# Kernel optimization log

Hardware: AMD Instinct MI355X
Metric: run time of the kernel (lower is better)

The kernel has to match this reference:

```python
import jax, jax.numpy as jnp
import numpy as np

RATIOS = [0.9, 0.7, 0.5, 0.3]
EPS = 1e-5


def _layernorm(x, g, b):
    m = jnp.mean(x, axis=-1, keepdims=True)
    v = jnp.mean(jnp.square(x - m), axis=-1, keepdims=True)
    return (x - m) * jax.lax.rsqrt(v + EPS) * g + b


def _stage(x, g, b, W, bias):
    return _layernorm(x, g, b) @ W + bias


def _prune(x, W1, b1, W2, b2, ratio):
    B, N, C = x.shape
    stats = jnp.mean(x, axis=1)                       # (B, C)
    scores = jax.nn.relu(stats @ W1 + b1) @ W2 + b2    # (B, C)
    k = max(1, int(C * ratio))
    _, idx = jax.lax.top_k(jax.lax.stop_gradient(scores), k)  # (B, k)
    hard = jnp.zeros((B, C), scores.dtype).at[jnp.arange(B)[:, None], idx].set(1.0)
    soft = jax.nn.sigmoid(scores)
    # straight-through: forward value == hard, gradient flows through soft
    mask = hard + soft - jax.lax.stop_gradient(soft)
    return x * mask[:, None, :]


def setup_inputs() -> dict:
    key = jax.random.key(0)
    dims = [(96, 96), (96, 192), (192, 384), (384, 768)]
    inp = {}
    ks = jax.random.split(key, 64)
    ki = iter(ks)
    inp["x"] = jax.random.normal(next(ki), (32, 3136, 96), dtype=jnp.float32)
    for i, (din, dout) in enumerate(dims, 1):
        inp[f"s{i}_g"] = jnp.ones((din,), jnp.float32)
        inp[f"s{i}_b"] = jnp.zeros((din,), jnp.float32)
        inp[f"s{i}_W"] = jax.random.normal(next(ki), (din, dout), jnp.float32) * 0.02
        inp[f"s{i}_bias"] = jnp.zeros((dout,), jnp.float32)
        d = dout
        inp[f"p{i}_W1"] = jax.random.normal(next(ki), (d, d // 4), jnp.float32) * 0.02
        inp[f"p{i}_b1"] = jnp.zeros((d // 4,), jnp.float32)
        inp[f"p{i}_W2"] = jax.random.normal(next(ki), (d // 4, d), jnp.float32) * 0.02
        inp[f"p{i}_b2"] = jnp.zeros((d,), jnp.float32)
    inp["H"] = 56
    inp["W"] = 56
    return inp


def reference(x,
              s1_g, s1_b, s1_W, s1_bias, p1_W1, p1_b1, p1_W2, p1_b2,
              s2_g, s2_b, s2_W, s2_bias, p2_W1, p2_b1, p2_W2, p2_b2,
              s3_g, s3_b, s3_W, s3_bias, p3_W1, p3_b1, p3_W2, p3_b2,
              s4_g, s4_b, s4_W, s4_bias, p4_W1, p4_b1, p4_W2, p4_b2,
              H, W):
    x = _stage(x, s1_g, s1_b, s1_W, s1_bias)
    x = _prune(x, p1_W1, p1_b1, p1_W2, p1_b2, RATIOS[0])
    x = _stage(x, s2_g, s2_b, s2_W, s2_bias)
    x = _prune(x, p2_W1, p2_b1, p2_W2, p2_b2, RATIOS[1])
    x = _stage(x, s3_g, s3_b, s3_W, s3_bias)
    x = _prune(x, p3_W1, p3_b1, p3_W2, p3_b2, RATIOS[2])
    x = _stage(x, s4_g, s4_b, s4_W, s4_bias)
    x = _prune(x, p4_W1, p4_b1, p4_W2, p4_b2, RATIOS[3])
    return x
```

## Files before the change

### kernel.cpp

```cpp
#include <hip/hip_runtime.h>
#include <hip/hip_bf16.h>
#include <stdint.h>

#define NTOK 3136
#define MTOT 100352
#define RPW  14
#define WPB  224

typedef __attribute__((ext_vector_type(8))) short bf16x8;
typedef __attribute__((ext_vector_type(4))) float f32x4;
typedef __attribute__((ext_vector_type(2))) float f32x2;

static __device__ __forceinline__ ushort f2bf(float x) {
  union { float f; uint32_t u; } c; c.f = x;
  uint32_t r = (c.u + 0x7FFFu + ((c.u >> 16) & 1u)) >> 16;
  return (ushort)r;
}
static __device__ __forceinline__ float bf2f(ushort h) {
  union { uint32_t u; float f; } c; c.u = ((uint32_t)h) << 16;
  return c.f;
}

template<int DIN, bool WLO>
__global__ __launch_bounds__(256)
void ln_colsum_k(const float* __restrict__ in, const float* __restrict__ gma,
                 const float* __restrict__ bta, ushort* __restrict__ oh,
                 ushort* __restrict__ ol, float* __restrict__ part)
{
  constexpr int P2 = DIN / 2;
  constexpr int T2 = (P2 + 63) / 64;
  const int wid  = (blockIdx.x * 256 + threadIdx.x) >> 6;
  const int lane = threadIdx.x & 63;
  const int b = wid / WPB;
  const int w = wid - b * WPB;

  f32x2 gv[T2], bv[T2], acc[T2];
#pragma unroll
  for (int t = 0; t < T2; ++t) {
    int c2 = lane + 64 * t;
    if (c2 < P2) {
      gv[t] = *(const f32x2*)(gma + 2 * c2);
      bv[t] = *(const f32x2*)(bta + 2 * c2);
    } else { gv[t] = {0.f, 0.f}; bv[t] = {0.f, 0.f}; }
    acc[t] = {0.f, 0.f};
  }

  const size_t rbase = ((size_t)b * NTOK + (size_t)w * RPW) * DIN;
  const float* ip = in + rbase;
  ushort* oph = oh + rbase;
  ushort* opl = ol + rbase;

  for (int j = 0; j < RPW; ++j) {
    f32x2 v[T2];
    float s = 0.f, sq = 0.f;
#pragma unroll
    for (int t = 0; t < T2; ++t) {
      int c2 = lane + 64 * t;
      f32x2 xv = {0.f, 0.f};
      if (c2 < P2) xv = *(const f32x2*)(ip + (size_t)j * DIN + 2 * c2);
      v[t] = xv;
      s  += xv[0] + xv[1];
      sq += xv[0] * xv[0] + xv[1] * xv[1];
    }
#pragma unroll
    for (int off = 1; off < 64; off <<= 1) {
      s  += __shfl_xor(s, off);
      sq += __shfl_xor(sq, off);
    }
    float m   = s / (float)DIN;
    float var = sq / (float)DIN - m * m;
    float r   = 1.f / sqrtf(var + 1e-5f);
#pragma unroll
    for (int t = 0; t < T2; ++t) {
      int c2 = lane + 64 * t;
      if (c2 < P2) {
        float xn0 = (v[t][0] - m) * r * gv[t][0] + bv[t][0];
        float xn1 = (v[t][1] - m) * r * gv[t][1] + bv[t][1];
        ushort h0 = f2bf(xn0), h1 = f2bf(xn1);
        ((uint32_t*)(oph + (size_t)j * DIN))[c2] =
            (uint32_t)h0 | ((uint32_t)h1 << 16);
        if (WLO) {
          ushort l0 = f2bf(xn0 - bf2f(h0)), l1 = f2bf(xn1 - bf2f(h1));
          ((uint32_t*)(opl + (size_t)j * DIN))[c2] =
              (uint32_t)l0 | ((uint32_t)l1 << 16);
        }
        acc[t][0] += xn0;
        acc[t][1] += xn1;
      }
    }
  }
#pragma unroll
  for (int t = 0; t < T2; ++t) {
    int c2 = lane + 64 * t;
    if (c2 < P2) {
      int c = 2 * c2;
      part[((size_t)b * DIN + c) * WPB + w]     = acc[t][0];
      part[((size_t)b * DIN + c + 1) * WPB + w] = acc[t][1];
    }
  }
}

template<int DIN, int DOUT, int SLOTS, bool CMP>
__global__ __launch_bounds__(1024)
void scores_k(const float* __restrict__ part,
              const float* __restrict__ Wt, const float* __restrict__ bias,
              const float* __restrict__ W1, const float* __restrict__ b1,
              const float* __restrict__ W2, const float* __restrict__ b2,
              float* __restrict__ mask, int k,
              const ushort* __restrict__ wsrc, ushort* __restrict__ wc,
              int* __restrict__ list_g, float* __restrict__ biasc)
{
  constexpr int DH  = DOUT / 4;
  constexpr int DH4 = DH / 4;
  constexpr int NSLC = (1024 / DH4 < 64) ? 1024 / DH4 : 64;
  constexpr int RPSC = (DOUT + NSLC - 1) / NSLC;
  constexpr int C4  = DOUT / 4;
  constexpr int NSLD = (1024 / C4 < 64) ? 1024 / C4 : 64;
  constexpr int RPSD = (DH + NSLD - 1) / NSLD;

  __shared__ float xm[DIN];
  __shared__ float st[DOUT];
  __shared__ float h[DH];
  __shared__ float sc[DOUT];
  __shared__ float red[4096];
  __shared__ int lsh[256];

  const int b = blockIdx.x, tid = threadIdx.x;

  if constexpr (SLOTS == 25) {
    if (tid < DIN) {
      const float* p = part + ((size_t)b * DIN + tid) * 25;
      float s = 0.f;
#pragma unroll
      for (int i = 0; i < 25; ++i) s += p[i];
      xm[tid] = s * (1.f / (float)NTOK);
    }
  } else {
    const int cg = tid >> 2, wq = tid & 3;
    if (cg < DIN) {
      const float* p = part + ((size_t)b * DIN + cg) * WPB + wq * 56;
      f32x4 a = {0.f, 0.f, 0.f, 0.f};
#pragma unroll
      for (int u = 0; u < 14; ++u) {
        f32x4 t0 = *(const f32x4*)(p + u * 4);
        a[0] += t0[0]; a[1] += t0[1]; a[2] += t0[2]; a[3] += t0[3];
      }
      red[wq * DIN + cg] = (a[0] + a[1]) + (a[2] + a[3]);
    }
    __syncthreads();
    if (tid < DIN)
      xm[tid] = ((red[0 * DIN + tid] + red[1 * DIN + tid]) +
                 (red[2 * DIN + tid] + red[3 * DIN + tid])) * (1.f / (float)NTOK);
  }
  __syncthreads();

  {
    constexpr int RPS = DIN / 4;
    const int j4 = tid % C4, sl = tid / C4;
    if (sl < 4) {
      const float* wp = Wt + (size_t)(sl * RPS) * DOUT + j4 * 4;
      f32x4 acc = {0.f, 0.f, 0.f, 0.f};
#pragma unroll
      for (int r = 0; r < RPS; ++r) {
        f32x4 wv = *(const f32x4*)(wp + (size_t)r * DOUT);
        float xv = xm[sl * RPS + r];
        acc[0] = fmaf(xv, wv[0], acc[0]);
        acc[1] = fmaf(xv, wv[1], acc[1]);
        acc[2] = fmaf(xv, wv[2], acc[2]);
        acc[3] = fmaf(xv, wv[3], acc[3]);
      }
      *(f32x4*)&red[sl * DOUT + j4 * 4] = acc;
    }
  }
  __syncthreads();
  if (tid < DOUT)
    st[tid] = ((red[0 * DOUT + tid] + red[1 * DOUT + tid]) +
               (red[2 * DOUT + tid] + red[3 * DOUT + tid])) + bias[tid];
  __syncthreads();

  {
    const int j4 = tid % DH4, sl = tid / DH4;
    if (sl < NSLC) {
      f32x4 acc = {0.f, 0.f, 0.f, 0.f};
#pragma unroll
      for (int rr = 0; rr < RPSC; ++rr) {
        int r = sl * RPSC + rr;
        if (r < DOUT) {
          f32x4 wv = *(const f32x4*)(W1 + (size_t)r * DH + j4 * 4);
          float sv = st[r];
          acc[0] = fmaf(sv, wv[0], acc[0]);
          acc[1] = fmaf(sv, wv[1], acc[1]);
          acc[2] = fmaf(sv, wv[2], acc[2]);
          acc[3] = fmaf(sv, wv[3], acc[3]);
        }
      }
      *(f32x4*)&red[(size_t)sl * DH + j4 * 4] = acc;
    }
  }
  __syncthreads();
  if (tid < DH) {
    float a = 0.f;
#pragma unroll 4
    for (int sl = 0; sl < NSLC; ++sl) a += red[(size_t)sl * DH + tid];
    h[tid] = fmaxf(b1[tid] + a, 0.f);
  }
  __syncthreads();

  {
    const int c4 = tid % C4, sl = tid / C4;
    if (sl < NSLD) {
      f32x4 acc = {0.f, 0.f, 0.f, 0.f};
#pragma unroll
      for (int rr = 0; rr < RPSD; ++rr) {
        int r = sl * RPSD + rr;
        if (r < DH) {
          f32x4 wv = *(const f32x4*)(W2 + (size_t)r * DOUT + c4 * 4);
          float hv = h[r];
          acc[0] = fmaf(hv, wv[0], acc[0]);
          acc[1] = fmaf(hv, wv[1], acc[1]);
          acc[2] = fmaf(hv, wv[2], acc[2]);
          acc[3] = fmaf(hv, wv[3], acc[3]);
        }
      }
      *(f32x4*)&red[(size_t)sl * DOUT + c4 * 4] = acc;
    }
  }
  __syncthreads();
  for (int c = tid; c < DOUT; c += 1024) {
    float a = 0.f;
#pragma unroll 4
    for (int sl = 0; sl < NSLD; ++sl) a += red[(size_t)sl * DOUT + c];
    sc[c] = b2[c] + a;
  }
  __syncthreads();

  for (int c = tid; c < DOUT; c += 1024) {
    float v = sc[c];
    int rank = 0;
#pragma unroll 8
    for (int j = 0; j < DOUT; ++j) {
      float u = sc[j];
      rank += (u > v) || (u == v && j < c);
    }
    mask[(size_t)b * DOUT + c] = (rank < k) ? 1.f : 0.f;
    if (CMP && rank < k) lsh[rank] = c;
  }
  if constexpr (CMP) {
    if (tid >= k && tid < 256) lsh[tid] = -1;
    __syncthreads();
    if (tid < 256) {
      int c = lsh[tid];
      list_g[b * 256 + tid] = c;
      biasc[b * 256 + tid] = (c >= 0) ? bias[c] : 0.f;
    }
    constexpr int U4 = 384 / 8;
    for (int idx = tid; idx < 256 * U4; idx += 1024) {
      int j = idx / U4, u = idx - j * U4;
      int src = lsh[j];
      uint4 v = make_uint4(0u, 0u, 0u, 0u);
      if (src >= 0) v = *(const uint4*)(wsrc + (size_t)src * 384 + u * 8);
      *(uint4*)(wc + (size_t)b * 98304 + (size_t)j * 384 + u * 8) = v;
    }
  }
}

__global__ __launch_bounds__(256)
void convW_all_k(const float* __restrict__ W0, const float* __restrict__ W1,
                 const float* __restrict__ W2, const float* __restrict__ W3,
                 ushort* __restrict__ hi, ushort* __restrict__ lo)
{
  const int Kd[4]   = { 96, 96, 192, 384 };
  const int Nd[4]   = { 96, 192, 384, 768 };
  const int off[5]  = { 0, 12288, 36864, 110592, 405504 };
  const float* Wp[4] = { W0, W1, W2, W3 };

  int idx = blockIdx.x * 256 + threadIdx.x;
  if (idx >= 405504) return;
  int s = (idx >= off[1]) + (idx >= off[2]) + (idx >= off[3]);
  int local = idx - off[s];
  int K = Kd[s], N = Nd[s];
  int n = local / K, kk = local - n * K;
  float v = (n < N) ? Wp[s][(size_t)kk * N + n] : 0.f;
  ushort h = f2bf(v);
  hi[idx] = h;
  lo[idx] = f2bf(v - bf2f(h));
}

#define ASYNC16(GP, LP) __builtin_amdgcn_global_load_lds( \
    (const __attribute__((address_space(1))) void*)(GP),  \
    (__attribute__((address_space(3))) void*)(LP), 16, 0, 0)

template<int K, int NSEG, int BNL, int N, int NWN, bool WLO>
__global__ __launch_bounds__(128 * NWN)
void gemm_ln_k(const ushort* __restrict__ a0, const ushort* __restrict__ a1,
               const ushort* __restrict__ a2,
               const ushort* __restrict__ b0, const ushort* __restrict__ b1,
               const ushort* __restrict__ b2,
               const float* __restrict__ bias, const float* __restrict__ msk,
               const float* __restrict__ gnext, const float* __restrict__ bnext,
               ushort* __restrict__ oh, ushort* __restrict__ ol,
               float* __restrict__ part)
{
  constexpr int T   = 128 * NWN;
  constexpr int R   = T / 4;
  constexpr int AI  = 128 / R;
  constexpr int BI  = BNL / R;
  constexpr int IS  = AI + BI;
  constexpr int WN  = N / NWN;
  constexpr int NFR = WN / 16;
  constexpr int KSTEPS = K / 32;
  constexpr int NT  = NSEG * KSTEPS;
  __shared__ __align__(16) ushort ldsA[3][128 * 32];
  __shared__ __align__(16) ushort ldsB[3][BNL * 32];

  const int tid  = threadIdx.x;
  const int lane = tid & 63;
  const int wid  = tid >> 6;
  const int wm = wid & 1, wn = wid >> 1;

  const int q8  = gridDim.x >> 3;
  const int bid = blockIdx.x;
  const int mt  = (bid & 7) * q8 + (bid >> 3);
  const size_t row0 = (size_t)mt * 128;

  const ushort* Aseg[3] = { a0, a1, a2 };
  const ushort* Bseg[3] = { b0, b1, b2 };

  f32x4 acc[4][NFR];
#pragma unroll
  for (int i = 0; i < 4; ++i)
#pragma unroll
    for (int j = 0; j < NFR; ++j) acc[i][j] = { 0.f, 0.f, 0.f, 0.f };

  const int c_row  = tid >> 2;
  const int c_phys = tid & 3;

#define STAGEF(BUF, TT)                                                        \
  {                                                                            \
    const int seg_ = (TT) / KSTEPS;                                            \
    const int k0_  = ((TT) % KSTEPS) * 32;                                     \
    const ushort* ap_ = Aseg[seg_];                                            \
    const ushort* bp_ = Bseg[seg_];                                            \
    _Pragma("unroll")                                                          \
    for (int r_ = 0; r_ < AI; ++r_) {                                          \
      int row_  = c_row + r_ * R;                                              \
      int slot_ = c_phys ^ ((row_ >> 1) & 3);                                  \
      ASYNC16(ap_ + (row0 + row_) * (size_t)K + (k0_ + slot_ * 8),             \
              &ldsA[BUF][(row_ * 4 + c_phys) * 8]);                            \
    }                                                                          \
    _Pragma("unroll")                                                          \
    for (int r_ = 0; r_ < BI; ++r_) {                                          \
      int row_  = c_row + r_ * R;                                              \
      int slot_ = c_phys ^ ((row_ >> 1) & 3);                                  \
      ASYNC16(bp_ + (size_t)row_ * K + (k0_ + slot_ * 8),                      \
              &ldsB[BUF][(row_ * 4 + c_phys) * 8]);                            \
    }                                                                          \
  }

  STAGEF(0, 0);
  STAGEF(1, 1);
#pragma unroll
  for (int t = 0; t < NT; ++t) {
    if (t == NT - 1)            { asm volatile("s_waitcnt vmcnt(0)" ::: "memory"); }
    else if constexpr (IS == 4) { asm volatile("s_waitcnt vmcnt(4)" ::: "memory"); }
    else                        { asm volatile("s_waitcnt vmcnt(5)" ::: "memory"); }
    __builtin_amdgcn_s_barrier();
    if (t + 2 < NT) STAGEF((t + 2) % 3, t + 2);
    const int buf = t % 3;
    const int slot = lane >> 4;
    const int r16  = lane & 15;
    bf16x8 af[4], bfr[NFR];
#pragma unroll
    for (int mi = 0; mi < 4; ++mi) {
      int r = wm * 64 + mi * 16 + r16;
      af[mi] = *(const bf16x8*)&ldsA[buf][(r * 4 + (slot ^ ((r >> 1) & 3))) * 8];
    }
#pragma unroll
    for (int ni = 0; ni < NFR; ++ni) {
      int r = wn * WN + ni * 16 + r16;
      bfr[ni] = *(const bf16x8*)&ldsB[buf][(r * 4 + (slot ^ ((r >> 1) & 3))) * 8];
    }
#pragma unroll
    for (int mi = 0; mi < 4; ++mi)
#pragma unroll
      for (int ni = 0; ni < NFR; ++ni)
        acc[mi][ni] = __builtin_amdgcn_mfma_f32_16x16x32_bf16(af[mi], bfr[ni],
                                                              acc[mi][ni], 0, 0, 0);
  }
#undef STAGEF

  __syncthreads();

  float* rowred = (float*)&ldsA[0][0];
  ushort* xsh = (ushort*)&ldsB[0][0];
  ushort* xsl = xsh + 32 * N;
  float* colred = (float*)(xsh + 32 * N * (WLO ? 2 : 1));

  const int l15 = lane & 15, l4 = lane >> 4;
  const int b0i = (int)(row0 / NTOK);
  const size_t rowB = (size_t)(b0i + 1) * NTOK;
  const bool strad = rowB < row0 + 128;

  float biasv[NFR], mk0a[NFR], mk1a[NFR], gvn[NFR], bvn[NFR];
#pragma unroll
  for (int ni = 0; ni < NFR; ++ni) {
    int n = wn * WN + ni * 16 + l15;
    biasv[ni] = bias[n];
    mk0a[ni] = msk[(size_t)b0i * N + n];
    mk1a[ni] = strad ? msk[(size_t)(b0i + 1) * N + n] : mk0a[ni];
    gvn[ni] = gnext[n];
    bvn[ni] = bnext[n];
  }

  float rs[16], rq[16];
#pragma unroll
  for (int i = 0; i < 16; ++i) { rs[i] = 0.f; rq[i] = 0.f; }
#pragma unroll
  for (int mi = 0; mi < 4; ++mi)
#pragma unroll
    for (int q = 0; q < 4; ++q) {
      size_t row = row0 + wm * 64 + mi * 16 + l4 * 4 + q;
      bool loB = row < rowB;
#pragma unroll
      for (int ni = 0; ni < NFR; ++ni) {
        float v = (acc[mi][ni][q] + biasv[ni]) * (loB ? mk0a[ni] : mk1a[ni]);
        acc[mi][ni][q] = v;
        rs[mi * 4 + q] += v;
        rq[mi * 4 + q] += v * v;
      }
    }
#pragma unroll
  for (int off = 1; off < 16; off <<= 1)
#pragma unroll
    for (int i = 0; i < 16; ++i) {
      rs[i] += __shfl_xor(rs[i], off);
      rq[i] += __shfl_xor(rq[i], off);
    }
  if (l15 == 0) {
#pragma unroll
    for (int mi = 0; mi < 4; ++mi)
#pragma unroll
      for (int q = 0; q < 4; ++q) {
        int r = wm * 64 + mi * 16 + l4 * 4 + q;
        rowred[(wn * 128 + r) * 2 + 0] = rs[mi * 4 + q];
        rowred[(wn * 128 + r) * 2 + 1] = rq[mi * 4 + q];
      }
  }
  __syncthreads();

  float mean[16], rstd[16];
#pragma unroll
  for (int mi = 0; mi < 4; ++mi)
#pragma unroll
    for (int q = 0; q < 4; ++q) {
      int r = wm * 64 + mi * 16 + l4 * 4 + q;
      float S = 0.f, Q = 0.f;
#pragma unroll
      for (int w = 0; w < NWN; ++w) {
        S += rowred[(w * 128 + r) * 2 + 0];
        Q += rowred[(w * 128 + r) * 2 + 1];
      }
      float mn  = S / (float)N;
      float var = Q / (float)N - mn * mn;
      mean[mi * 4 + q] = mn;
      rstd[mi * 4 + q] = 1.f / sqrtf(var + 1e-5f);
    }

  float cs0[NFR], cs1[NFR];
#pragma unroll
  for (int ni = 0; ni < NFR; ++ni) { cs0[ni] = 0.f; cs1[ni] = 0.f; }
#pragma unroll
  for (int mi = 0; mi < 4; ++mi) {
    __syncthreads();
#pragma unroll
    for (int q = 0; q < 4; ++q) {
      const int rl = l4 * 4 + q;
      const size_t row = row0 + wm * 64 + mi * 16 + rl;
      const bool loB = row < rowB;
      const float mn = mean[mi * 4 + q], rv = rstd[mi * 4 + q];
#pragma unroll
      for (int ni = 0; ni < NFR; ++ni) {
        const int n = wn * WN + ni * 16 + l15;
        float xn = (acc[mi][ni][q] - mn) * rv * gvn[ni] + bvn[ni];
        ushort hh = f2bf(xn);
        xsh[(wm * 16 + rl) * N + n] = hh;
        if constexpr (WLO) xsl[(wm * 16 + rl) * N + n] = f2bf(xn - bf2f(hh));
        if (loB) cs0[ni] += xn; else cs1[ni] += xn;
      }
    }
    __syncthreads();
    constexpr int U4R = N / 8;
    for (int idx = tid; idx < 32 * U4R; idx += T) {
      const int grp = idx / U4R, c = idx - grp * U4R;
      const size_t row = row0 + (grp >> 4) * 64 + mi * 16 + (grp & 15);
      *(uint4*)(oh + row * (size_t)N + c * 8) =
          *(const uint4*)(xsh + grp * N + c * 8);
      if constexpr (WLO)
        *(uint4*)(ol + row * (size_t)N + c * 8) =
            *(const uint4*)(xsl + grp * N + c * 8);
    }
  }

#pragma unroll
  for (int ni = 0; ni < NFR; ++ni) {
    cs0[ni] += __shfl_xor(cs0[ni], 16);
    cs0[ni] += __shfl_xor(cs0[ni], 32);
    cs1[ni] += __shfl_xor(cs1[ni], 16);
    cs1[ni] += __shfl_xor(cs1[ni], 32);
  }
  __syncthreads();
  if (l4 == 0) {
#pragma unroll
    for (int ni = 0; ni < NFR; ++ni) {
      int n = wn * WN + ni * 16 + l15;
      colred[(0 * 2 + wm) * N + n] = cs0[ni];
      colred[(1 * 2 + wm) * N + n] = cs1[ni];
    }
  }
  __syncthreads();
  if (wm == 0 && l4 == 0) {
    const int mt_lo = (b0i * NTOK) >> 7;
    const int slot0 = mt - mt_lo;
#pragma unroll
    for (int ni = 0; ni < NFR; ++ni) {
      int n = wn * WN + ni * 16 + l15;
      float t0 = colred[0 * N + n] + colred[1 * N + n];
      part[((size_t)b0i * N + n) * 25 + slot0] = t0;
      if (strad) {
        float t1 = colred[2 * N + n] + colred[3 * N + n];
        part[((size_t)(b0i + 1) * N + n) * 25 + 0] = t1;
      }
    }
  }
}

template<int K>
__global__ __launch_bounds__(512)
void gemm_c4_k(const ushort* __restrict__ A, const ushort* __restrict__ Wc,
               const int* __restrict__ list, const float* __restrict__ biasc,
               float* __restrict__ C)
{
  constexpr int NT = K / 32;
  __shared__ __align__(16) ushort ldsA[3][128 * 32];
  __shared__ __align__(16) ushort ldsB[3][256 * 32];

  const int tid  = threadIdx.x;
  const int lane = tid & 63;
  const int wid  = tid >> 6;
  const int wm = wid & 1, wn = wid >> 1;

  const int q8  = gridDim.x >> 3;
  const int bid = blockIdx.x;
  const int wg  = (bid & 7) * q8 + (bid >> 3);
  const int b   = wg / 25;
  const int mt  = wg - b * 25;
  const size_t row0 = (size_t)b * NTOK + (size_t)mt * 128;
  const int rows_valid = (mt == 24) ? 64 : 128;

  const ushort* bp = Wc + (size_t)b * 256 * K;

  const int c_row  = tid >> 2;
  const int c_phys = tid & 3;

  size_t arow = row0 + c_row;
  const size_t rowEnd = (size_t)(b + 1) * NTOK;
  if (arow >= rowEnd) arow = rowEnd - 1;
  const ushort* apr = A + arow * (size_t)K;

  f32x4 acc[4][4];
#pragma unroll
  for (int i = 0; i < 4; ++i)
#pragma unroll
    for (int j = 0; j < 4; ++j) acc[i][j] = { 0.f, 0.f, 0.f, 0.f };

#define STAGEC(BUF, TT)                                                        \
  {                                                                            \
    const int k0_ = (TT) * 32;                                                 \
    {                                                                          \
      int slot_ = c_phys ^ ((c_row >> 1) & 3);                                 \
      ASYNC16(apr + (k0_ + slot_ * 8),                                         \
              &ldsA[BUF][(c_row * 4 + c_phys) * 8]);                           \
    }                                                                          \
    _Pragma("unroll")                                                          \
    for (int r_ = 0; r_ < 2; ++r_) {                                           \
      int row_  = c_row + r_ * 128;                                            \
      int slot_ = c_phys ^ ((row_ >> 1) & 3);                                  \
      ASYNC16(bp + (size_t)row_ * K + (k0_ + slot_ * 8),                       \
              &ldsB[BUF][(row_ * 4 + c_phys) * 8]);                            \
    }                                                                          \
  }

  STAGEC(0, 0);
  STAGEC(1, 1);
#pragma unroll
  for (int t = 0; t < NT; ++t) {
    if (t == NT - 1) { asm volatile("s_waitcnt vmcnt(0)" ::: "memory"); }
    else             { asm volatile("s_waitcnt vmcnt(3)" ::: "memory"); }
    __builtin_amdgcn_s_barrier();
    if (t + 2 < NT) STAGEC((t + 2) % 3, t + 2);
    const int buf = t % 3;
    const int slot = lane >> 4;
    const int r16  = lane & 15;
    bf16x8 af[4], bfr[4];
#pragma unroll
    for (int mi = 0; mi < 4; ++mi) {
      int r = wm * 64 + mi * 16 + r16;
      af[mi] = *(const bf16x8*)&ldsA[buf][(r * 4 + (slot ^ ((r >> 1) & 3))) * 8];
    }
#pragma unroll
    for (int ni = 0; ni < 4; ++ni) {
      int r = wn * 64 + ni * 16 + r16;
      bfr[ni] = *(const bf16x8*)&ldsB[buf][(r * 4 + (slot ^ ((r >> 1) & 3))) * 8];
    }
#pragma unroll
    for (int mi = 0; mi < 4; ++mi)
#pragma unroll
      for (int ni = 0; ni < 4; ++ni)
        acc[mi][ni] = __builtin_amdgcn_mfma_f32_16x16x32_bf16(af[mi], bfr[ni],
                                                              acc[mi][ni], 0, 0, 0);
  }
#undef STAGEC

  float* cst = (float*)&ldsB[0][0];

  const int l15 = lane & 15, l4 = lane >> 4;
  int   nj[4];
  float biasv[4];
#pragma unroll
  for (int ni = 0; ni < 4; ++ni) {
    int j = wn * 64 + ni * 16 + l15;
    nj[ni]    = list[b * 256 + j];
    biasv[ni] = biasc[b * 256 + j];
  }

#pragma unroll
  for (int hh = 0; hh < 8; ++hh) {
    const int hrows = rows_valid - hh * 16;
    if (hrows <= 0) break;
    __syncthreads();
    for (int idx = tid; idx < 16 * 192; idx += 512)
      ((f32x4*)cst)[idx] = f32x4{0.f, 0.f, 0.f, 0.f};
    __syncthreads();
    if ((hh >> 2) == wm) {
      const int mi = hh & 3;
#pragma unroll
      for (int q = 0; q < 4; ++q) {
        const int rl = l4 * 4 + q;
#pragma unroll
        for (int ni = 0; ni < 4; ++ni)
          if (nj[ni] >= 0)
            cst[rl * 768 + nj[ni]] = acc[mi][ni][q] + biasv[ni];
      }
    }
    __syncthreads();
    const int nst = (hrows >= 16 ? 16 : hrows) * 192;
    for (int idx = tid; idx < nst; idx += 512) {
      const int grp = idx / 192, c = idx - grp * 192;
      const size_t row = row0 + hh * 16 + grp;
      *(f32x4*)(C + row * 768 + c * 4) = ((const f32x4*)cst)[grp * 192 + c];
    }
  }
}

extern "C" void kernel_launch(void* const* d_in, const int* in_sizes, int n_in,
                              void* d_out, int out_size, void* d_ws, size_t ws_size,
                              hipStream_t stream)
{
  (void)in_sizes; (void)n_in; (void)out_size; (void)ws_size;
  const float* x = (const float*)d_in[0];
  const float *sg[4], *sb[4], *sW[4], *sbias[4], *pW1[4], *pb1[4], *pW2[4], *pb2[4];
  for (int s = 0; s < 4; ++s) {
    int base = 1 + s * 8;
    sg[s]    = (const float*)d_in[base + 0];
    sb[s]    = (const float*)d_in[base + 1];
    sW[s]    = (const float*)d_in[base + 2];
    sbias[s] = (const float*)d_in[base + 3];
    pW1[s]   = (const float*)d_in[base + 4];
    pb1[s]   = (const float*)d_in[base + 5];
    pW2[s]   = (const float*)d_in[base + 6];
    pb2[s]   = (const float*)d_in[base + 7];
  }

  float* out = (float*)d_out;
  ushort* hiA = (ushort*)out;
  ushort* loA = (ushort*)(out + 19267584);
  ushort* loB = (ushort*)(out + 38535168);

  char* ws = (char*)d_ws;
  ushort* hiB  = (ushort*)(ws);
  float*  part = (float*) (ws + 77070336);
  float*  mk   = (float*) (ws + 79822848);
  ushort* w_hi = (ushort*)(ws + 79921152);
  ushort* w_lo = (ushort*)(ws + 80732160);
  ushort* wc   = (ushort*)(ws + 81543168);
  int*    lst  = (int*)   (ws + 87834624);
  float*  bsc  = (float*) (ws + 87867392);

  const int woff[4] = { 0, 12288, 36864, 110592 };

  convW_all_k<<<(405504 + 255) / 256, 256, 0, stream>>>(
      sW[0], sW[1], sW[2], sW[3], w_hi, w_lo);

  const int LNG = 32 * WPB / 4;

  ln_colsum_k<96, true><<<LNG, 256, 0, stream>>>(x, sg[0], sb[0], hiA, loA, part);
  scores_k<96, 96, 224, false><<<32, 1024, 0, stream>>>(part, sW[0], sbias[0],
      pW1[0], pb1[0], pW2[0], pb2[0], mk, 86, nullptr, nullptr, nullptr, nullptr);
  gemm_ln_k<96, 3, 128, 96, 2, true><<<784, 256, 0, stream>>>(
      hiA, hiA, loA, w_hi + woff[0], w_lo + woff[0], w_hi + woff[0],
      sbias[0], mk, sg[1], sb[1], hiB, loB, part);

  scores_k<96, 192, 25, false><<<32, 1024, 0, stream>>>(part, sW[1], sbias[1],
      pW1[1], pb1[1], pW2[1], pb2[1], mk, 134, nullptr, nullptr, nullptr, nullptr);
  gemm_ln_k<96, 3, 192, 192, 2, true><<<784, 256, 0, stream>>>(
      hiB, hiB, loB, w_hi + woff[1], w_lo + woff[1], w_hi + woff[1],
      sbias[1], mk, sg[2], sb[2], hiA, loA, part);

  scores_k<192, 384, 25, false><<<32, 1024, 0, stream>>>(part, sW[2], sbias[2],
      pW1[2], pb1[2], pW2[2], pb2[2], mk, 192, nullptr, nullptr, nullptr, nullptr);
  gemm_ln_k<192, 3, 384, 384, 4, false><<<784, 512, 0, stream>>>(
      hiA, hiA, loA, w_hi + woff[2], w_lo + woff[2], w_hi + woff[2],
      sbias[2], mk, sg[3], sb[3], hiB, (ushort*)nullptr, part);

  scores_k<384, 768, 25, true><<<32, 1024, 0, stream>>>(part, sW[3], sbias[3],
      pW1[3], pb1[3], pW2[3], pb2[3], mk, 230, w_hi + woff[3], wc, lst, bsc);
  gemm_c4_k<384><<<800, 512, 0, stream>>>(hiB, wc, lst, bsc, out);
}
```

Baseline: 490.3 us.

## Compact stage-3 GEMM to surviving pruned channels with fused LayerNorm epilogue

Stage 3 now gathers only the k=192 selected output columns of the stage-3 weights (hi and lo bf16 splits) into per-batch compacted buffers inside the scores kernel. A new GEMM kernel computes just those columns and scatters them into the full 384-wide row for the next LayerNorm, writing zeros for pruned channels. This roughly halves stage-3 MFMA work and weight traffic. In exchange it adds a per-batch weight gather, an LDS scatter/zero-fill epilogue and a new 800-block grid with row clamping.

```diff
diff --git a/kernel.cpp b/kernel.cpp
--- a/kernel.cpp
+++ b/kernel.cpp
@@ -100,14 +100,15 @@
   }
 }
 
-template<int DIN, int DOUT, int SLOTS, bool CMP>
+template<int DIN, int DOUT, int SLOTS, bool CMP, int CMPN, int RLEN, bool GLO>
 __global__ __launch_bounds__(1024)
 void scores_k(const float* __restrict__ part,
               const float* __restrict__ Wt, const float* __restrict__ bias,
               const float* __restrict__ W1, const float* __restrict__ b1,
               const float* __restrict__ W2, const float* __restrict__ b2,
               float* __restrict__ mask, int k,
-              const ushort* __restrict__ wsrc, ushort* __restrict__ wc,
+              const ushort* __restrict__ whi, const ushort* __restrict__ wlo,
+              ushort* __restrict__ wch, ushort* __restrict__ wcl,
               int* __restrict__ list_g, float* __restrict__ biasc)
 {
   constexpr int DH  = DOUT / 4;
@@ -246,20 +247,25 @@
     if (CMP && rank < k) lsh[rank] = c;
   }
   if constexpr (CMP) {
-    if (tid >= k && tid < 256) lsh[tid] = -1;
+    if (tid >= k && tid < CMPN) lsh[tid] = -1;
     __syncthreads();
-    if (tid < 256) {
+    if (tid < CMPN) {
       int c = lsh[tid];
       list_g[b * 256 + tid] = c;
       biasc[b * 256 + tid] = (c >= 0) ? bias[c] : 0.f;
     }
-    constexpr int U4 = 384 / 8;
-    for (int idx = tid; idx < 256 * U4; idx += 1024) {
+    constexpr int U4 = RLEN / 8;
+    for (int idx = tid; idx < CMPN * U4; idx += 1024) {
       int j = idx / U4, u = idx - j * U4;
       int src = lsh[j];
       uint4 v = make_uint4(0u, 0u, 0u, 0u);
-      if (src >= 0) v = *(const uint4*)(wsrc + (size_t)src * 384 + u * 8);
-      *(uint4*)(wc + (size_t)b * 98304 + (size_t)j * 384 + u * 8) = v;
+      if (src >= 0) v = *(const uint4*)(whi + (size_t)src * RLEN + u * 8);
+      *(uint4*)(wch + ((size_t)b * CMPN + j) * RLEN + u * 8) = v;
+      if constexpr (GLO) {
+        uint4 vl = make_uint4(0u, 0u, 0u, 0u);
+        if (src >= 0) vl = *(const uint4*)(wlo + (size_t)src * RLEN + u * 8);
+        *(uint4*)(wcl + ((size_t)b * CMPN + j) * RLEN + u * 8) = vl;
+      }
     }
   }
 }
@@ -534,6 +540,239 @@
   }
 }
 
+template<int K, int NC, int N>
+__global__ __launch_bounds__(256)
+void gemm_lnc_k(const ushort* __restrict__ ahi, const ushort* __restrict__ alo,
+                const ushort* __restrict__ wch, const ushort* __restrict__ wcl,
+                const int* __restrict__ list, const float* __restrict__ biasc,
+                const float* __restrict__ gnext, const float* __restrict__ bnext,
+                ushort* __restrict__ oh, float* __restrict__ part)
+{
+  constexpr int KSTEPS = K / 32;
+  constexpr int NT  = 3 * KSTEPS;
+  constexpr int WN  = NC / 2;
+  constexpr int NFR = WN / 16;
+  __shared__ __align__(16) ushort ldsA[3][128 * 32];
+  __shared__ __align__(16) ushort ldsB[3][NC * 32];
+  __shared__ float rowred[2][128][2];
+  __shared__ float rowmnrv[128];
+  __shared__ float rowrv[128];
+
+  const int tid  = threadIdx.x;
+  const int lane = tid & 63;
+  const int wid  = tid >> 6;
+  const int wm = wid & 1, wn = wid >> 1;
+
+  const int q8  = gridDim.x >> 3;
+  const int bid = blockIdx.x;
+  const int wg  = (bid & 7) * q8 + (bid >> 3);
+  const int b   = wg / 25;
+  const int mt  = wg - b * 25;
+  const size_t row0 = (size_t)b * NTOK + (size_t)mt * 128;
+  const size_t rowEnd = (size_t)(b + 1) * NTOK;
+  const int rows_valid = (mt == 24) ? 64 : 128;
+
+  const ushort* Aseg[3] = { ahi, ahi, alo };
+  const ushort* Bseg[3] = { wch + (size_t)b * NC * K, wcl + (size_t)b * NC * K,
+                            wch + (size_t)b * NC * K };
+
+  f32x4 acc[4][NFR];
+#pragma unroll
+  for (int i = 0; i < 4; ++i)
+#pragma unroll
+    for (int j = 0; j < NFR; ++j) acc[i][j] = { 0.f, 0.f, 0.f, 0.f };
+
+  const int c_row  = tid >> 2;
+  const int c_phys = tid & 3;
+
+#define STAGEL(BUF, TT)                                                        \
+  {                                                                            \
+    const int seg_ = (TT) / KSTEPS;                                            \
+    const int k0_  = ((TT) % KSTEPS) * 32;                                     \
+    const ushort* ap_ = Aseg[seg_];                                            \
+    const ushort* bp_ = Bseg[seg_];                                            \
+    _Pragma("unroll")                                                          \
+    for (int r_ = 0; r_ < 2; ++r_) {                                           \
+      int row_  = c_row + r_ * 64;                                             \
+      int slot_ = c_phys ^ ((row_ >> 1) & 3);                                  \
+      size_t ar_ = row0 + row_;                                                \
+      if (ar_ >= rowEnd) ar_ = rowEnd - 1;                                     \
+      ASYNC16(ap_ + ar_ * (size_t)K + (k0_ + slot_ * 8),                       \
+              &ldsA[BUF][(row_ * 4 + c_phys) * 8]);                            \
+    }                                                                          \
+    _Pragma("unroll")                                                          \
+    for (int r_ = 0; r_ < 3; ++r_) {                                           \
+      int row_  = c_row + r_ * 64;                                             \
+      int slot_ = c_phys ^ ((row_ >> 1) & 3);                                  \
+      ASYNC16(bp_ + (size_t)row_ * K + (k0_ + slot_ * 8),                      \
+              &ldsB[BUF][(row_ * 4 + c_phys) * 8]);                            \
+    }                                                                          \
+  }
+
+  STAGEL(0, 0);
+  STAGEL(1, 1);
+#pragma unroll
+  for (int t = 0; t < NT; ++t) {
+    if (t == NT - 1) { asm volatile("s_waitcnt vmcnt(0)" ::: "memory"); }
+    else             { asm volatile("s_waitcnt vmcnt(5)" ::: "memory"); }
+    __builtin_amdgcn_s_barrier();
+    if (t + 2 < NT) STAGEL((t + 2) % 3, t + 2);
+    const int buf = t % 3;
+    const int slot = lane >> 4;
+    const int r16  = lane & 15;
+    bf16x8 af[4], bfr[NFR];
+#pragma unroll
+    for (int mi = 0; mi < 4; ++mi) {
+      int r = wm * 64 + mi * 16 + r16;
+      af[mi] = *(const bf16x8*)&ldsA[buf][(r * 4 + (slot ^ ((r >> 1) & 3))) * 8];
+    }
+#pragma unroll
+    for (int ni = 0; ni < NFR; ++ni) {
+      int r = wn * WN + ni * 16 + r16;
+      bfr[ni] = *(const bf16x8*)&ldsB[buf][(r * 4 + (slot ^ ((r >> 1) & 3))) * 8];
+    }
+#pragma unroll
+    for (int mi = 0; mi < 4; ++mi)
+#pragma unroll
+      for (int ni = 0; ni < NFR; ++ni)
+        acc[mi][ni] = __builtin_amdgcn_mfma_f32_16x16x32_bf16(af[mi], bfr[ni],
+                                                              acc[mi][ni], 0, 0, 0);
+  }
+#undef STAGEL
+
+  __syncthreads();
+
+  const int l15 = lane & 15, l4 = lane >> 4;
+
+  int   nj[NFR];
+  float biasv[NFR];
+#pragma unroll
+  for (int ni = 0; ni < NFR; ++ni) {
+    int j = wn * WN + ni * 16 + l15;
+    nj[ni]    = list[b * 256 + j];
+    biasv[ni] = biasc[b * 256 + j];
+  }
+
+  float rs[16], rq[16];
+#pragma unroll
+  for (int i = 0; i < 16; ++i) { rs[i] = 0.f; rq[i] = 0.f; }
+#pragma unroll
+  for (int mi = 0; mi < 4; ++mi)
+#pragma unroll
+    for (int q = 0; q < 4; ++q) {
+#pragma unroll
+      for (int ni = 0; ni < NFR; ++ni) {
+        float v = acc[mi][ni][q] + biasv[ni];
+        acc[mi][ni][q] = v;
+        rs[mi * 4 + q] += v;
+        rq[mi * 4 + q] += v * v;
+      }
+    }
+#pragma unroll
+  for (int off = 1; off < 16; off <<= 1)
+#pragma unroll
+    for (int i = 0; i < 16; ++i) {
+      rs[i] += __shfl_xor(rs[i], off);
+      rq[i] += __shfl_xor(rq[i], off);
+    }
+  if (l15 == 0) {
+#pragma unroll
+    for (int mi = 0; mi < 4; ++mi)
+#pragma unroll
+      for (int q = 0; q < 4; ++q) {
+        int r = wm * 64 + mi * 16 + l4 * 4 + q;
+        rowred[wn][r][0] = rs[mi * 4 + q];
+        rowred[wn][r][1] = rq[mi * 4 + q];
+      }
+  }
+  __syncthreads();
+  if (tid < 128) {
+    float S = rowred[0][tid][0] + rowred[1][tid][0];
+    float Q = rowred[0][tid][1] + rowred[1][tid][1];
+    float mn = S / (float)N;
+    float rv = 1.f / sqrtf(Q / (float)N - mn * mn + 1e-5f);
+    rowmnrv[tid] = mn * rv;
+    rowrv[tid]   = rv;
+  }
+  __syncthreads();
+
+  float* sbuf = (float*)&ldsB[0][0];
+  float colS = 0.f, colS2 = 0.f;
+
+#pragma unroll
+  for (int h = 0; h < 8; ++h) {
+    if (h * 16 >= rows_valid) break;
+    __syncthreads();
+    for (int idx = tid; idx < 16 * N / 4; idx += 256)
+      ((f32x4*)sbuf)[idx] = f32x4{0.f, 0.f, 0.f, 0.f};
+    __syncthreads();
+    if ((h >> 2) == wm) {
+      const int mi = h & 3;
+#pragma unroll
+      for (int q = 0; q < 4; ++q) {
+        const int rl = l4 * 4 + q;
+        const float rv = rowrv[h * 16 + rl];
+#pragma unroll
+        for (int ni = 0; ni < NFR; ++ni)
+          sbuf[rl * N + nj[ni]] = acc[mi][ni][q] * rv;
+      }
+    }
+    __syncthreads();
+    {
+      float a = 0.f;
+#pragma unroll
+      for (int rl = 0; rl < 16; ++rl) a += sbuf[rl * N + tid];
+      colS += a;
+      if (tid < N - 256) {
+        float a2 = 0.f;
+        const int c2 = 256 + tid;
+#pragma unroll
+        for (int rl = 0; rl < 16; ++rl) a2 += sbuf[rl * N + c2];
+        colS2 += a2;
+      }
+    }
+    for (int idx = tid; idx < 16 * (N / 8); idx += 256) {
+      const int rl = idx / (N / 8), cg = idx - rl * (N / 8);
+      const float mnrv = rowmnrv[h * 16 + rl];
+      const float* sp = sbuf + rl * N + cg * 8;
+      f32x4 s0 = *(const f32x4*)(sp);
+      f32x4 s1 = *(const f32x4*)(sp + 4);
+      f32x4 g0 = *(const f32x4*)(gnext + cg * 8);
+      f32x4 g1 = *(const f32x4*)(gnext + cg * 8 + 4);
+      f32x4 e0 = *(const f32x4*)(bnext + cg * 8);
+      f32x4 e1 = *(const f32x4*)(bnext + cg * 8 + 4);
+      uint32_t w[4];
+#pragma unroll
+      for (int j = 0; j < 2; ++j) {
+        ushort ha = f2bf(g0[2*j]   * (s0[2*j]   - mnrv) + e0[2*j]);
+        ushort hb = f2bf(g0[2*j+1] * (s0[2*j+1] - mnrv) + e0[2*j+1]);
+        w[j] = (uint32_t)ha | ((uint32_t)hb << 16);
+      }
+#pragma unroll
+      for (int j = 0; j < 2; ++j) {
+        ushort ha = f2bf(g1[2*j]   * (s1[2*j]   - mnrv) + e1[2*j]);
+        ushort hb = f2bf(g1[2*j+1] * (s1[2*j+1] - mnrv) + e1[2*j+1]);
+        w[2 + j] = (uint32_t)ha | ((uint32_t)hb << 16);
+      }
+      *(uint4*)(oh + (row0 + h * 16 + rl) * (size_t)N + cg * 8) =
+          make_uint4(w[0], w[1], w[2], w[3]);
+    }
+  }
+
+  float msum = 0.f;
+  for (int r = 0; r < rows_valid; ++r) msum += rowmnrv[r];
+  {
+    const int c = tid;
+    part[((size_t)b * N + c) * 25 + mt] =
+        gnext[c] * (colS - msum) + (float)rows_valid * bnext[c];
+    if (tid < N - 256) {
+      const int c2 = 256 + tid;
+      part[((size_t)b * N + c2) * 25 + mt] =
+          gnext[c2] * (colS2 - msum) + (float)rows_valid * bnext[c2];
+    }
+  }
+}
+
 template<int K>
 __global__ __launch_bounds__(512)
 void gemm_c4_k(const ushort* __restrict__ A, const ushort* __restrict__ Wc,
@@ -696,6 +935,9 @@
   int*    lst  = (int*)   (ws + 87834624);
   float*  bsc  = (float*) (ws + 87867392);
 
+  ushort* wch3 = wc;
+  ushort* wcl3 = wc + 1179648;
+
   const int woff[4] = { 0, 12288, 36864, 110592 };
 
   convW_all_k<<<(405504 + 255) / 256, 256, 0, stream>>>(
@@ -704,25 +946,28 @@
   const int LNG = 32 * WPB / 4;
 
   ln_colsum_k<96, true><<<LNG, 256, 0, stream>>>(x, sg[0], sb[0], hiA, loA, part);
-  scores_k<96, 96, 224, false><<<32, 1024, 0, stream>>>(part, sW[0], sbias[0],
-      pW1[0], pb1[0], pW2[0], pb2[0], mk, 86, nullptr, nullptr, nullptr, nullptr);
+  scores_k<96, 96, 224, false, 256, 384, false><<<32, 1024, 0, stream>>>(
+      part, sW[0], sbias[0], pW1[0], pb1[0], pW2[0], pb2[0], mk, 86,
+      nullptr, nullptr, nullptr, nullptr, nullptr, nullptr);
   gemm_ln_k<96, 3, 128, 96, 2, true><<<784, 256, 0, stream>>>(
       hiA, hiA, loA, w_hi + woff[0], w_lo + woff[0], w_hi + woff[0],
       sbias[0], mk, sg[1], sb[1], hiB, loB, part);
 
-  scores_k<96, 192, 25, false><<<32, 1024, 0, stream>>>(part, sW[1], sbias[1],
-      pW1[1], pb1[1], pW2[1], pb2[1], mk, 134, nullptr, nullptr, nullptr, nullptr);
+  scores_k<96, 192, 25, false, 256, 384, false><<<32, 1024, 0, stream>>>(
+      part, sW[1], sbias[1], pW1[1], pb1[1], pW2[1], pb2[1], mk, 134,
+      nullptr, nullptr, nullptr, nullptr, nullptr, nullptr);
   gemm_ln_k<96, 3, 192, 192, 2, true><<<784, 256, 0, stream>>>(
       hiB, hiB, loB, w_hi + woff[1], w_lo + woff[1], w_hi + woff[1],
       sbias[1], mk, sg[2], sb[2], hiA, loA, part);
 
-  scores_k<192, 384, 25, false><<<32, 1024, 0, stream>>>(part, sW[2], sbias[2],
-      pW1[2], pb1[2], pW2[2], pb2[2], mk, 192, nullptr, nullptr, nullptr, nullptr);
-  gemm_ln_k<192, 3, 384, 384, 4, false><<<784, 512, 0, stream>>>(
-      hiA, hiA, loA, w_hi + woff[2], w_lo + woff[2], w_hi + woff[2],
-      sbias[2], mk, sg[3], sb[3], hiB, (ushort*)nullptr, part);
-
-  scores_k<384, 768, 25, true><<<32, 1024, 0, stream>>>(part, sW[3], sbias[3],
-      pW1[3], pb1[3], pW2[3], pb2[3], mk, 230, w_hi + woff[3], wc, lst, bsc);
+  scores_k<192, 384, 25, true, 192, 192, true><<<32, 1024, 0, stream>>>(
+      part, sW[2], sbias[2], pW1[2], pb1[2], pW2[2], pb2[2], mk, 192,
+      w_hi + woff[2], w_lo + woff[2], wch3, wcl3, lst, bsc);
+  gemm_lnc_k<192, 192, 384><<<800, 256, 0, stream>>>(
+      hiA, loA, wch3, wcl3, lst, bsc, sg[3], sb[3], hiB, part);
+
+  scores_k<384, 768, 25, true, 256, 384, false><<<32, 1024, 0, stream>>>(
+      part, sW[3], sbias[3], pW1[3], pb1[3], pW2[3], pb2[3], mk, 230,
+      w_hi + woff[3], nullptr, wc, nullptr, lst, bsc);
   gemm_c4_k<384><<<800, 512, 0, stream>>>(hiB, wc, lst, bsc, out);
 }
```

Measured after the change: 475.8 us. 3.0% less time.
